# Optimization experiments

Measured on AMD Instinct MI355X. Metric: run time of the kernel, lower is better.

The kernel has to match this reference:

```python
import jax, jax.numpy as jnp
import numpy as np
from jax import lax

BETA = 5.0
THRESHOLD = 20.0

def softplus5(x):
    # torch nn.Softplus(beta=5, threshold=20)
    return jnp.where(BETA * x > THRESHOLD, x, jax.nn.softplus(BETA * x) / BETA)

def setup_inputs() -> dict:
    key = jax.random.key(0)
    k1, k2, k3, k4, k5 = jax.random.split(key, 5)
    B, T, I, H = 128, 256, 1024, 1024
    stdv = 1.0 / np.sqrt(H)
    x = jax.random.normal(k1, (B, T, I), dtype=jnp.float32)
    hidden = jnp.zeros((2, B, H), dtype=jnp.float32)
    Wi = jax.random.uniform(k2, (H, I), dtype=jnp.float32, minval=-stdv, maxval=stdv)
    bi = jax.random.uniform(k3, (H,), dtype=jnp.float32, minval=-stdv, maxval=stdv)
    Wh = jax.random.uniform(k4, (H, H), dtype=jnp.float32, minval=-stdv, maxval=stdv)
    bh = jax.random.uniform(k5, (H,), dtype=jnp.float32, minval=-stdv, maxval=stdv)
    return {"x": x, "hidden": hidden, "Wi": Wi, "bi": bi, "Wh": Wh, "bh": bh}

def reference(x, hidden, Wi, bi, Wh, bh):
    # x: [B, T, I] (batch_first) -> time-major [T, B, I]
    xt = jnp.swapaxes(x, 0, 1)
    T = xt.shape[0]
    # precompute i2h for all steps (one big GEMM)
    pre = jnp.einsum('tbi,hi->tbh', xt, Wi) + bi  # [T, B, H]

    def step(h, p):
        h_next = softplus5(p + h @ Wh.T + bh)
        return h_next, h_next

    _, fwd = lax.scan(step, hidden[0], pre)          # fwd[t]: hidden after step t
    _, bwd = lax.scan(step, hidden[1], pre[::-1])    # bwd[j]: backward hidden at time i = T-1-j
    # bi_outputs appended for i = T-1 ... 0: position t holds cat(outputs[(T-1-t)-16], bwd[t])
    idx = (jnp.arange(T)[::-1] - 16) % T  # Python negative-index wrap of outputs[i-16]
    out = jnp.concatenate([fwd[idx], bwd], axis=-1)  # [T, B, 2H]
    return jnp.swapaxes(out, 0, 1)                   # [B, T, 2H]
```

## Files before the change

kernel.cpp:

```cpp
#include <hip/hip_runtime.h>
#include <stddef.h>

using short8 = __attribute__((ext_vector_type(8))) short;
using f32x4  = __attribute__((ext_vector_type(4))) float;
using f32x16 = __attribute__((ext_vector_type(16))) float;
using u16x4  = __attribute__((ext_vector_type(4))) unsigned short;

__device__ __forceinline__ unsigned short cvt_bf16(float f) {
    unsigned u = __builtin_bit_cast(unsigned, f);
    u += 0x7fffu + ((u >> 16) & 1u);
    return (unsigned short)(u >> 16);
}

__device__ __forceinline__ void gload_lds16(const void* g, void* l) {
    __builtin_amdgcn_global_load_lds(
        (const __attribute__((address_space(1))) unsigned*)g,
        (__attribute__((address_space(3))) unsigned*)l, 16, 0, 0);
}

#define MFMA16(a, b, c) __builtin_amdgcn_mfma_f32_16x16x32_bf16((a), (b), (c), 0, 0, 0)
#define MFMA32(a, b, c) __builtin_amdgcn_mfma_f32_32x32x16_bf16((a), (b), (c), 0, 0, 0)

struct SyncCell {
    unsigned counter; unsigned pad0[31];
    unsigned epoch;   unsigned pad1[31];
};

__global__ __launch_bounds__(256) void convert_w(const float* __restrict__ Wi,
                                                 const float* __restrict__ Wh,
                                                 unsigned short* __restrict__ Wib,
                                                 unsigned short* __restrict__ Whb) {
    const float* src = blockIdx.y ? Wh : Wi;
    unsigned short* dst = blockIdx.y ? Whb : Wib;
    int base = blockIdx.x * 2048 + threadIdx.x * 8;
#pragma unroll
    for (int c = 0; c < 2; ++c) {
        float4 v = *(const float4*)(src + base + c * 4);
        u16x4 o;
        o.x = cvt_bf16(v.x); o.y = cvt_bf16(v.y); o.z = cvt_bf16(v.z); o.w = cvt_bf16(v.w);
        *(u16x4*)(dst + base + c * 4) = o;
    }
}

__global__ __launch_bounds__(256) void init_h(const float* __restrict__ hidden,
                                              unsigned short* __restrict__ h0,
                                              unsigned* __restrict__ syncw) {
    int row = blockIdx.x;
    int tid = threadIdx.x;
    float4 v = *(const float4*)(hidden + (size_t)row * 1024 + tid * 4);
    u16x4 o;
    o.x = cvt_bf16(v.x); o.y = cvt_bf16(v.y); o.z = cvt_bf16(v.z); o.w = cvt_bf16(v.w);
    *(u16x4*)(h0 + (size_t)row * 1024 + tid * 4) = o;
    if (blockIdx.x == 0) {
        for (int i = tid; i < 512; i += 256) syncw[i] = 0;
    }
}

__global__ __launch_bounds__(256) void pre_gemm(const float* __restrict__ x,
                                                const unsigned short* __restrict__ Wib,
                                                const float* __restrict__ bi,
                                                float* __restrict__ pre) {
    __shared__ unsigned short Alds[128 * 64];
    __shared__ unsigned short Blds[128 * 64];
    const int tid  = threadIdx.x;
    const int lane = tid & 63, wid = tid >> 6;
    const int wr = wid >> 1, wc = wid & 1;
    const int t  = blockIdx.y;
    const int n0 = blockIdx.x * 128;

    f32x4 acc[4][4] = {};

    for (int kt = 0; kt < 16; ++kt) {
        const int k0 = kt * 64;
        __syncthreads();
#pragma unroll
        for (int c = 0; c < 8; ++c) {
            int flat = c * 256 + tid;
            int row = flat >> 4;
            int seg = flat & 15;
            float4 v = *(const float4*)(x + (size_t)row * 262144 + (size_t)t * 1024 + k0 + seg * 4);
            u16x4 h;
            h.x = cvt_bf16(v.x); h.y = cvt_bf16(v.y); h.z = cvt_bf16(v.z); h.w = cvt_bf16(v.w);
            *(u16x4*)&Alds[row * 64 + seg * 4] = h;
        }
#pragma unroll
        for (int c = 0; c < 4; ++c) {
            int flat = c * 256 + tid;
            int row = flat >> 3;
            int seg = flat & 7;
            gload_lds16(Wib + (size_t)(n0 + row) * 1024 + k0 + seg * 8, &Blds[flat * 8]);
        }
        __syncthreads();
#pragma unroll
        for (int ks = 0; ks < 2; ++ks) {
            short8 a[4], b[4];
#pragma unroll
            for (int i = 0; i < 4; ++i)
                a[i] = *(const short8*)&Alds[(wr * 64 + i * 16 + (lane & 15)) * 64 + ks * 32 + (lane >> 4) * 8];
#pragma unroll
            for (int j = 0; j < 4; ++j)
                b[j] = *(const short8*)&Blds[(wc * 64 + j * 16 + (lane & 15)) * 64 + ks * 32 + (lane >> 4) * 8];
#pragma unroll
            for (int i = 0; i < 4; ++i)
#pragma unroll
                for (int j = 0; j < 4; ++j)
                    acc[i][j] = MFMA16(a[i], b[j], acc[i][j]);
        }
    }
    const int rbase = wr * 64 + (lane >> 4) * 4;
    const int cbase = n0 + wc * 64 + (lane & 15);
#pragma unroll
    for (int i = 0; i < 4; ++i) {
#pragma unroll
        for (int j = 0; j < 4; ++j) {
            int n = cbase + j * 16;
            float bv = bi[n];
#pragma unroll
            for (int r = 0; r < 4; ++r) {
                int m = rbase + i * 16 + r;
                pre[((size_t)t * 128 + m) * 1024 + n] = acc[i][j][r] + bv;
            }
        }
    }
}

__global__ __launch_bounds__(256, 1) void rnn_scan(const unsigned short* __restrict__ Whb,
                                                   const float* __restrict__ pre,
                                                   const float* __restrict__ bh,
                                                   unsigned short* __restrict__ ha,
                                                   unsigned short* __restrict__ hb,
                                                   float* __restrict__ out,
                                                   SyncCell* __restrict__ sync) {
    __shared__ unsigned short Alds[32 * 1024];
    __shared__ float Red[4][1024];

    const int tid  = threadIdx.x;
    const int lane = tid & 63, wid = tid >> 6;
    const int bid  = blockIdx.x;
    const int g    = bid & 7, ni = bid >> 3;
    const int m0   = g * 32, n0 = ni * 32;
    const bool fwd = (g < 4);

    short8 bfrag[16];
    {
        const unsigned short* bp = Whb + (size_t)(n0 + (lane & 31)) * 1024
                                 + wid * 256 + (lane >> 5) * 8;
#pragma unroll
        for (int ks = 0; ks < 16; ++ks)
            bfrag[ks] = *(const short8*)(bp + ks * 16);
    }

    const int mloc = tid >> 3;
    const int nloc = (tid & 7) * 4;
    const int m    = m0 + mloc;
    const int b    = m & 127;
    const int n    = n0 + nloc;
    const float4 bh4 = *(const float4*)(bh + n);
    float* outp      = out + (size_t)b * 524288 + (fwd ? 0 : 1024) + n;
    const float* prebase = pre + (size_t)b * 1024 + n;
    unsigned* ep  = &sync[g].epoch;
    unsigned* cnt = &sync[g].counter;

    const char* aswz_base = (const char*)Alds + (lane & 31) * 2048;
    const int   aswz      = (lane & 7) << 4;
    const int   kb0       = wid * 512 + (lane >> 5) * 16;

    for (int s = 0; s < 256; ++s) {
        const unsigned short* hin = (s & 1) ? hb : ha;
        unsigned short* hout      = (s & 1) ? ha : hb;
        const int prow = fwd ? s : 255 - s;
        float4 pv = *(const float4*)(prebase + (size_t)prow * 131072);

        if (s > 0 && tid == 0) {
            int fuel = 1 << 22;
            while (__hip_atomic_load(ep, __ATOMIC_RELAXED, __HIP_MEMORY_SCOPE_AGENT) < (unsigned)s
                   && --fuel)
                __builtin_amdgcn_s_sleep(1);
        }
        __syncthreads();

        {
            const unsigned long long* hsrc =
                (const unsigned long long*)(hin + (size_t)m0 * 1024);
            const int colswz = tid * 8;
#pragma unroll
            for (int ph = 0; ph < 2; ++ph) {
                unsigned long long tmp[16];
#pragma unroll
                for (int i = 0; i < 16; ++i)
                    tmp[i] = __hip_atomic_load(&hsrc[(size_t)(ph * 16 + i) * 256 + tid],
                                               __ATOMIC_RELAXED, __HIP_MEMORY_SCOPE_AGENT);
#pragma unroll
                for (int i = 0; i < 16; ++i) {
                    int row = ph * 16 + i;
                    *(unsigned long long*)((char*)Alds + row * 2048
                                           + (colswz ^ ((row & 7) << 4))) = tmp[i];
                }
            }
        }
        __syncthreads();

        f32x16 acc0 = {}, acc1 = {};
#pragma unroll
        for (int ks = 0; ks < 16; ++ks) {
            short8 a = *(const short8*)(aswz_base + ((kb0 + ks * 32) ^ aswz));
            if (ks & 1) acc1 = MFMA32(a, bfrag[ks], acc1);
            else        acc0 = MFMA32(a, bfrag[ks], acc0);
        }
        f32x16 acc = acc0 + acc1;
#pragma unroll
        for (int r = 0; r < 16; ++r) {
            int row = (r & 3) + 8 * (r >> 2) + 4 * (lane >> 5);
            Red[wid][row * 32 + (lane & 31)] = acc[r];
        }
        __syncthreads();

        {
            const int o = tid * 4;
            float4 q0 = *(const float4*)&Red[0][o];
            float4 q1 = *(const float4*)&Red[1][o];
            float4 q2 = *(const float4*)&Red[2][o];
            float4 q3 = *(const float4*)&Red[3][o];
            float vv[4] = { q0.x + q1.x + q2.x + q3.x + pv.x + bh4.x,
                            q0.y + q1.y + q2.y + q3.y + pv.y + bh4.y,
                            q0.z + q1.z + q2.z + q3.z + pv.z + bh4.z,
                            q0.w + q1.w + q2.w + q3.w + pv.w + bh4.w };
            f32x4 ov;
            u16x4 hh;
#pragma unroll
            for (int j = 0; j < 4; ++j) {
                float xv = vv[j];
                float hv = (5.0f * xv > 20.0f) ? xv : 0.2f * log1pf(__expf(5.0f * xv));
                ov[j] = hv;
                hh[j] = cvt_bf16(hv);
            }
            __hip_atomic_store((unsigned long long*)(hout + (size_t)m * 1024 + n),
                               __builtin_bit_cast(unsigned long long, hh),
                               __ATOMIC_RELAXED, __HIP_MEMORY_SCOPE_AGENT);
            int tout = fwd ? ((239 - s) & 255) : s;
            __builtin_nontemporal_store(ov, (f32x4*)(outp + (size_t)tout * 2048));
        }
        asm volatile("s_waitcnt vmcnt(0)" ::: "memory");
        __syncthreads();

        if (s < 255 && tid == 0) {
            unsigned c = __hip_atomic_fetch_add(cnt, 1u, __ATOMIC_RELAXED,
                                                __HIP_MEMORY_SCOPE_AGENT);
            if (c == (unsigned)(32 * (s + 1) - 1))
                __hip_atomic_store(ep, (unsigned)(s + 1), __ATOMIC_RELAXED,
                                   __HIP_MEMORY_SCOPE_AGENT);
        }
    }
}

extern "C" void kernel_launch(void* const* d_in, const int* in_sizes, int n_in,
                              void* d_out, int out_size, void* d_ws, size_t ws_size,
                              hipStream_t stream) {
    const float* x      = (const float*)d_in[0];
    const float* hidden = (const float*)d_in[1];
    const float* Wi     = (const float*)d_in[2];
    const float* bi     = (const float*)d_in[3];
    const float* Wh     = (const float*)d_in[4];
    const float* bh     = (const float*)d_in[5];
    float* out = (float*)d_out;

    char* ws = (char*)d_ws;
    float*          pre = (float*)ws;
    unsigned short* Wib = (unsigned short*)(ws + 134217728);
    unsigned short* Whb = (unsigned short*)(ws + 136314880);
    unsigned short* ha  = (unsigned short*)(ws + 138412032);
    unsigned short* hb  = (unsigned short*)(ws + 138936320);
    SyncCell*      sync = (SyncCell*)(ws + 139460608);

    convert_w<<<dim3(512, 2), 256, 0, stream>>>(Wi, Wh, Wib, Whb);
    init_h<<<256, 256, 0, stream>>>(hidden, ha, (unsigned*)sync);
    pre_gemm<<<dim3(8, 256), 256, 0, stream>>>(x, Wib, bi, pre);
    rnn_scan<<<256, 256, 0, stream>>>(Whb, pre, bh, ha, hb, out, sync);
}
```

Baseline: 1.444 ms.

## Replace counter/epoch barrier with per-block flags and move output store past signal

```diff
diff --git a/kernel.cpp b/kernel.cpp
--- a/kernel.cpp
+++ b/kernel.cpp
@@ -20,11 +20,6 @@
 
 #define MFMA16(a, b, c) __builtin_amdgcn_mfma_f32_16x16x32_bf16((a), (b), (c), 0, 0, 0)
 #define MFMA32(a, b, c) __builtin_amdgcn_mfma_f32_32x32x16_bf16((a), (b), (c), 0, 0, 0)
-
-struct SyncCell {
-    unsigned counter; unsigned pad0[31];
-    unsigned epoch;   unsigned pad1[31];
-};
 
 __global__ __launch_bounds__(256) void convert_w(const float* __restrict__ Wi,
                                                  const float* __restrict__ Wh,
@@ -44,16 +39,14 @@
 
 __global__ __launch_bounds__(256) void init_h(const float* __restrict__ hidden,
                                               unsigned short* __restrict__ h0,
-                                              unsigned* __restrict__ syncw) {
+                                              unsigned* __restrict__ flags) {
     int row = blockIdx.x;
     int tid = threadIdx.x;
     float4 v = *(const float4*)(hidden + (size_t)row * 1024 + tid * 4);
     u16x4 o;
     o.x = cvt_bf16(v.x); o.y = cvt_bf16(v.y); o.z = cvt_bf16(v.z); o.w = cvt_bf16(v.w);
     *(u16x4*)(h0 + (size_t)row * 1024 + tid * 4) = o;
-    if (blockIdx.x == 0) {
-        for (int i = tid; i < 512; i += 256) syncw[i] = 0;
-    }
+    if (blockIdx.x == 0 && tid < 256) flags[tid] = 0;
 }
 
 __global__ __launch_bounds__(256) void pre_gemm(const float* __restrict__ x,
@@ -130,7 +123,7 @@
                                                    unsigned short* __restrict__ ha,
                                                    unsigned short* __restrict__ hb,
                                                    float* __restrict__ out,
-                                                   SyncCell* __restrict__ sync) {
+                                                   unsigned* __restrict__ flags) {
     __shared__ unsigned short Alds[32 * 1024];
     __shared__ float Red[4][1024];
 
@@ -140,6 +133,7 @@
     const int g    = bid & 7, ni = bid >> 3;
     const int m0   = g * 32, n0 = ni * 32;
     const bool fwd = (g < 4);
+    unsigned* gflags = flags + g * 32;
 
     short8 bfrag[16];
     {
@@ -158,8 +152,6 @@
     const float4 bh4 = *(const float4*)(bh + n);
     float* outp      = out + (size_t)b * 524288 + (fwd ? 0 : 1024) + n;
     const float* prebase = pre + (size_t)b * 1024 + n;
-    unsigned* ep  = &sync[g].epoch;
-    unsigned* cnt = &sync[g].counter;
 
     const char* aswz_base = (const char*)Alds + (lane & 31) * 2048;
     const int   aswz      = (lane & 7) << 4;
@@ -171,32 +163,31 @@
         const int prow = fwd ? s : 255 - s;
         float4 pv = *(const float4*)(prebase + (size_t)prow * 131072);
 
-        if (s > 0 && tid == 0) {
-            int fuel = 1 << 22;
-            while (__hip_atomic_load(ep, __ATOMIC_RELAXED, __HIP_MEMORY_SCOPE_AGENT) < (unsigned)s
-                   && --fuel)
-                __builtin_amdgcn_s_sleep(1);
-        }
-        __syncthreads();
+        if (s > 0) {
+            if (tid < 64) {
+                int fuel = 1 << 20;
+                unsigned v;
+                do {
+                    v = __hip_atomic_load(&gflags[lane & 31], __ATOMIC_RELAXED,
+                                          __HIP_MEMORY_SCOPE_AGENT);
+                } while (!__all((int)(v >= (unsigned)s)) && --fuel);
+            }
+            __syncthreads();
+        }
 
         {
             const unsigned long long* hsrc =
                 (const unsigned long long*)(hin + (size_t)m0 * 1024);
             const int colswz = tid * 8;
-#pragma unroll
-            for (int ph = 0; ph < 2; ++ph) {
-                unsigned long long tmp[16];
-#pragma unroll
-                for (int i = 0; i < 16; ++i)
-                    tmp[i] = __hip_atomic_load(&hsrc[(size_t)(ph * 16 + i) * 256 + tid],
-                                               __ATOMIC_RELAXED, __HIP_MEMORY_SCOPE_AGENT);
-#pragma unroll
-                for (int i = 0; i < 16; ++i) {
-                    int row = ph * 16 + i;
-                    *(unsigned long long*)((char*)Alds + row * 2048
-                                           + (colswz ^ ((row & 7) << 4))) = tmp[i];
-                }
-            }
+            unsigned long long tmp[32];
+#pragma unroll
+            for (int i = 0; i < 32; ++i)
+                tmp[i] = __hip_atomic_load(&hsrc[(size_t)i * 256 + tid],
+                                           __ATOMIC_RELAXED, __HIP_MEMORY_SCOPE_AGENT);
+#pragma unroll
+            for (int i = 0; i < 32; ++i)
+                *(unsigned long long*)((char*)Alds + i * 2048
+                                       + (colswz ^ ((i & 7) << 4))) = tmp[i];
         }
         __syncthreads();
 
@@ -215,6 +206,7 @@
         }
         __syncthreads();
 
+        f32x4 ov;
         {
             const int o = tid * 4;
             float4 q0 = *(const float4*)&Red[0][o];
@@ -225,7 +217,6 @@
                             q0.y + q1.y + q2.y + q3.y + pv.y + bh4.y,
                             q0.z + q1.z + q2.z + q3.z + pv.z + bh4.z,
                             q0.w + q1.w + q2.w + q3.w + pv.w + bh4.w };
-            f32x4 ov;
             u16x4 hh;
 #pragma unroll
             for (int j = 0; j < 4; ++j) {
@@ -237,19 +228,16 @@
             __hip_atomic_store((unsigned long long*)(hout + (size_t)m * 1024 + n),
                                __builtin_bit_cast(unsigned long long, hh),
                                __ATOMIC_RELAXED, __HIP_MEMORY_SCOPE_AGENT);
-            int tout = fwd ? ((239 - s) & 255) : s;
-            __builtin_nontemporal_store(ov, (f32x4*)(outp + (size_t)tout * 2048));
         }
         asm volatile("s_waitcnt vmcnt(0)" ::: "memory");
         __syncthreads();
 
-        if (s < 255 && tid == 0) {
-            unsigned c = __hip_atomic_fetch_add(cnt, 1u, __ATOMIC_RELAXED,
-                                                __HIP_MEMORY_SCOPE_AGENT);
-            if (c == (unsigned)(32 * (s + 1) - 1))
-                __hip_atomic_store(ep, (unsigned)(s + 1), __ATOMIC_RELAXED,
-                                   __HIP_MEMORY_SCOPE_AGENT);
-        }
+        if (s < 255 && tid == 0)
+            __hip_atomic_store(&gflags[ni], (unsigned)(s + 1),
+                               __ATOMIC_RELAXED, __HIP_MEMORY_SCOPE_AGENT);
+
+        int tout = fwd ? ((239 - s) & 255) : s;
+        __builtin_nontemporal_store(ov, (f32x4*)(outp + (size_t)tout * 2048));
     }
 }
 
@@ -270,10 +258,10 @@
     unsigned short* Whb = (unsigned short*)(ws + 136314880);
     unsigned short* ha  = (unsigned short*)(ws + 138412032);
     unsigned short* hb  = (unsigned short*)(ws + 138936320);
-    SyncCell*      sync = (SyncCell*)(ws + 139460608);
+    unsigned*     flags = (unsigned*)(ws + 139460608);
 
     convert_w<<<dim3(512, 2), 256, 0, stream>>>(Wi, Wh, Wib, Whb);
-    init_h<<<256, 256, 0, stream>>>(hidden, ha, (unsigned*)sync);
+    init_h<<<256, 256, 0, stream>>>(hidden, ha, flags);
     pre_gemm<<<dim3(8, 256), 256, 0, stream>>>(x, Wib, bi, pre);
-    rnn_scan<<<256, 256, 0, stream>>>(Whb, pre, bh, ha, hb, out, sync);
-}
+    rnn_scan<<<256, 256, 0, stream>>>(Whb, pre, bh, ha, hb, out, flags);
+}
```

Result: faster. 1.214 ms (-15.9%).
